# Optimization experiments

Measured on AMD Instinct MI355X. Metric: run time of the kernel, lower is better.

The kernel has to match this reference:

```python
import jax, jax.numpy as jnp
import numpy as np

EPS = 1e-12  # F.normalize eps


def setup_inputs() -> dict:
    key = jax.random.key(0)
    k1, k2, k3, k4 = jax.random.split(key, 4)
    D, K, H, W = 256, 64, 512, 512
    x = jax.random.normal(k1, (1, D, H, W), dtype=jnp.float32)
    c = jax.random.normal(k2, (K, D), dtype=jnp.float32)
    conv_w = jax.random.normal(k3, (K, D), dtype=jnp.float32) * (1.0 / np.sqrt(D))
    conv_b = jax.random.normal(k4, (K,), dtype=jnp.float32) * 0.01
    return {"x": x, "c": c, "conv_w": conv_w, "conv_b": conv_b}


def reference(x, c, conv_w, conv_b):
    # x: (1, D, H, W); base_cnn treated as identity (feature map given directly)
    _, D, H, W = x.shape
    K = conv_w.shape[0]
    N = H * W
    xf = x.reshape(D, N)                                  # (D, N) local descriptors

    # 1x1 conv soft-assignment: logits (K, N), softmax over clusters K
    logits = jnp.einsum('kd,dn->kn', conv_w, xf) + conv_b[:, None]
    a_bar = jax.nn.softmax(logits, axis=0)                # (K, N)

    # VLAD core (vectorized): V[k] = sum_n a_bar[k,n] * (x[:,n] - c[k])
    V = jnp.einsum('kn,dn->kd', a_bar, xf) - c * a_bar.sum(axis=1, keepdims=True)  # (K, D)

    # intra-normalization over cluster axis (dim=0), then per-row L2 (F.normalize default dim=1)
    V = V / jnp.maximum(jnp.linalg.norm(V, axis=0, keepdims=True), EPS)
    y = V / jnp.maximum(jnp.linalg.norm(V, axis=1, keepdims=True), EPS)
    return y
```

## Files before the change

### kernel.cpp

```cpp
#include <hip/hip_runtime.h>
#include <hip/hip_bf16.h>

#define DD    256
#define KK    64
#define NPIX  262144
#define NW    128
#define NWIN  8
#define GRID  256
#define BLOCK 512

#define W_S   264
#define XT_S  132
#define AB_S  136
#define XC_S  40
#define SV_S  257

typedef __attribute__((ext_vector_type(8))) short bf16x8;
typedef __attribute__((ext_vector_type(4))) float f32x4;

union Frag { bf16x8 v; int i[4]; };

__device__ __forceinline__ int cvtpk(float a, float b) {
    __hip_bfloat162 h = __float22bfloat162_rn(float2{a, b});
    int r; __builtin_memcpy(&r, &h, 4); return r;
}

__device__ __forceinline__ void lds_barrier() {
    asm volatile("s_waitcnt lgkmcnt(0)" ::: "memory");
    __builtin_amdgcn_s_barrier();
}

__global__ __attribute__((amdgpu_flat_work_group_size(BLOCK, BLOCK), amdgpu_waves_per_eu(2, 2)))
void netvlad_fused(const float* __restrict__ x, const float* __restrict__ conv_w,
                   const float* __restrict__ conv_b, float* __restrict__ Vpart,
                   float* __restrict__ asum_part)
{
    __shared__ short Wl[KK * W_S];
    __shared__ short Ab[KK * AB_S];
    __shared__ float asb[8][KK];
    __shared__ short slice_mem[8 * 16 * XC_S];
    __shared__ union {
        short xt[DD * XT_S];
        float sv[KK * SV_S];
    } UX;

    const int t    = threadIdx.x;
    const int lane = t & 63;
    const int w    = t >> 6;
    const int l15  = lane & 15;
    const int q    = (lane >> 4) & 3;
    const int bid  = blockIdx.x;
    const size_t n0 = (size_t)bid * (NWIN * NW);

    const int p  = lane >> 2;
    const int ng = lane & 3;
    const size_t nself0 = n0 + 16 * w + 4 * ng;

    float4 pr[4][2];
    #pragma unroll
    for (int c = 0; c < 2; ++c)
        #pragma unroll
        for (int j = 0; j < 2; ++j)
            pr[c][j] = *(const float4*)(x + (size_t)(32 * c + 2 * p + j) * NPIX + nself0);
    __builtin_amdgcn_sched_barrier(0);

    #pragma unroll
    for (int i = 0; i < 32; ++i) {
        int idx = t + BLOCK * i;
        float wv = conv_w[idx];
        __hip_bfloat16 hb = __float2bfloat16(wv);
        short s; __builtin_memcpy(&s, &hb, 2);
        Wl[(idx >> 8) * W_S + (idx & 255)] = s;
    }

    #pragma unroll
    for (int c = 2; c < 4; ++c)
        #pragma unroll
        for (int j = 0; j < 2; ++j)
            pr[c][j] = *(const float4*)(x + (size_t)(32 * c + 2 * p + j) * NPIX + nself0);
    __builtin_amdgcn_sched_barrier(0);

    float breg[4][4];
    #pragma unroll
    for (int mt = 0; mt < 4; ++mt)
        #pragma unroll
        for (int r = 0; r < 4; ++r)
            breg[mt][r] = conv_b[16 * mt + 4 * q + r];

    f32x4 acc[2][4];
    #pragma unroll
    for (int rg = 0; rg < 2; ++rg)
        #pragma unroll
        for (int ct = 0; ct < 4; ++ct)
            acc[rg][ct] = (f32x4){0.f, 0.f, 0.f, 0.f};
    float asumReg = 0.f;

    short* slice = &slice_mem[w * (16 * XC_S)];

    lds_barrier();

    for (int i = 0; i < NWIN; ++i) {
        const size_t nselfw = n0 + (size_t)i * NW + 16 * w + 4 * ng;

        f32x4 Lc[4];
        #pragma unroll
        for (int mt = 0; mt < 4; ++mt) Lc[mt] = (f32x4){0.f, 0.f, 0.f, 0.f};

        #pragma unroll
        for (int ch = 0; ch < 8; ++ch) {
            const int cur = ch & 3;
            const float* r0 = (const float*)&pr[cur][0];
            const float* r1 = (const float*)&pr[cur][1];

            #pragma unroll
            for (int c = 0; c < 4; ++c) {
                int pk = cvtpk(r0[c], r1[c]);
                *(int*)&slice[(4 * ng + c) * XC_S + 2 * p] = pk;
            }
            {
                int2 a; a.x = cvtpk(r0[0], r0[1]); a.y = cvtpk(r0[2], r0[3]);
                *(int2*)&UX.xt[(32 * ch + 2 * p) * XT_S + 16 * w + 4 * ng] = a;
                int2 b; b.x = cvtpk(r1[0], r1[1]); b.y = cvtpk(r1[2], r1[3]);
                *(int2*)&UX.xt[(32 * ch + 2 * p + 1) * XT_S + 16 * w + 4 * ng] = b;
            }

            if (ch < 4) {
                #pragma unroll
                for (int j = 0; j < 2; ++j)
                    pr[cur][j] = *(const float4*)(x + (size_t)(32 * (ch + 4) + 2 * p + j) * NPIX + nselfw);
                __builtin_amdgcn_sched_barrier(0);
            } else if (i + 1 < NWIN) {
                #pragma unroll
                for (int j = 0; j < 2; ++j)
                    pr[cur][j] = *(const float4*)(x + (size_t)(32 * (ch - 4) + 2 * p + j) * NPIX + nselfw + NW);
                __builtin_amdgcn_sched_barrier(0);
            }

            Frag Bv = *(const Frag*)&slice[l15 * XC_S + 8 * q];
            #pragma unroll
            for (int mt = 0; mt < 4; ++mt) {
                Frag A = *(const Frag*)&Wl[(16 * mt + l15) * W_S + 32 * ch + 8 * q];
                Lc[mt] = __builtin_amdgcn_mfma_f32_16x16x32_bf16(A.v, Bv.v, Lc[mt], 0, 0, 0);
            }
        }

        {
            float mx = -1e30f;
            #pragma unroll
            for (int mt = 0; mt < 4; ++mt)
                #pragma unroll
                for (int r = 0; r < 4; ++r) {
                    Lc[mt][r] += breg[mt][r];
                    mx = fmaxf(mx, Lc[mt][r]);
                }
            mx = fmaxf(mx, __shfl_xor(mx, 16));
            mx = fmaxf(mx, __shfl_xor(mx, 32));
            float s = 0.f;
            #pragma unroll
            for (int mt = 0; mt < 4; ++mt)
                #pragma unroll
                for (int r = 0; r < 4; ++r) {
                    float e = __expf(Lc[mt][r] - mx);
                    Lc[mt][r] = e;
                    s += e;
                }
            s += __shfl_xor(s, 16);
            s += __shfl_xor(s, 32);
            float inv = 1.0f / s;
            #pragma unroll
            for (int mt = 0; mt < 4; ++mt)
                #pragma unroll
                for (int r = 0; r < 4; ++r)
                    Lc[mt][r] *= inv;
        }

        #pragma unroll
        for (int mt = 0; mt < 4; ++mt)
            #pragma unroll
            for (int r = 0; r < 4; ++r) {
                float v = Lc[mt][r];
                v += __shfl_xor(v, 1);
                v += __shfl_xor(v, 2);
                v += __shfl_xor(v, 4);
                v += __shfl_xor(v, 8);
                if (l15 == 0) asb[w][16 * mt + 4 * q + r] = v;
            }

        #pragma unroll
        for (int mt = 0; mt < 4; ++mt)
            #pragma unroll
            for (int r = 0; r < 4; ++r) {
                __hip_bfloat16 hb = __float2bfloat16(Lc[mt][r]);
                short sv_; __builtin_memcpy(&sv_, &hb, 2);
                Ab[(16 * mt + 4 * q + r) * AB_S + 16 * w + l15] = sv_;
            }

        lds_barrier();

        if (t < KK) {
            float s = 0.f;
            #pragma unroll
            for (int ww = 0; ww < 8; ++ww) s += asb[ww][t];
            asumReg += s;
        }

        #pragma unroll
        for (int s = 0; s < 4; ++s) {
            Frag Af0 = *(const Frag*)&UX.xt[(32 * w + l15) * XT_S + 32 * s + 8 * q];
            Frag Af1 = *(const Frag*)&UX.xt[(32 * w + 16 + l15) * XT_S + 32 * s + 8 * q];
            Frag Bf[4];
            #pragma unroll
            for (int ct = 0; ct < 4; ++ct)
                Bf[ct] = *(const Frag*)&Ab[(16 * ct + l15) * AB_S + 32 * s + 8 * q];
            #pragma unroll
            for (int ct = 0; ct < 4; ++ct) {
                acc[0][ct] = __builtin_amdgcn_mfma_f32_16x16x32_bf16(Af0.v, Bf[ct].v, acc[0][ct], 0, 0, 0);
                acc[1][ct] = __builtin_amdgcn_mfma_f32_16x16x32_bf16(Af1.v, Bf[ct].v, acc[1][ct], 0, 0, 0);
            }
        }

        lds_barrier();
    }

    if (t < KK) asum_part[(size_t)bid * KK + t] = asumReg;

    #pragma unroll
    for (int rg = 0; rg < 2; ++rg)
        #pragma unroll
        for (int ct = 0; ct < 4; ++ct)
            #pragma unroll
            for (int r = 0; r < 4; ++r) {
                int k = 16 * ct + l15;
                int d = 32 * w + 16 * rg + 4 * q + r;
                UX.sv[k * SV_S + d] = acc[rg][ct][r];
            }
    __syncthreads();

    float* vout = Vpart + (size_t)bid * (KK * DD);
    #pragma unroll
    for (int ii = 0; ii < 32; ++ii) {
        int idx = t + BLOCK * ii;
        vout[idx] = UX.sv[(idx >> 8) * SV_S + (idx & 255)];
    }
}

__global__ __launch_bounds__(256)
void netvlad_reduce(const float* __restrict__ Vpart, const float* __restrict__ asum_part,
                    float* __restrict__ Vred, float* __restrict__ asum_red)
{
    __shared__ float sbuf[256];
    const int t = threadIdx.x;
    if (blockIdx.x < 256) {
        const int o = blockIdx.x * 64 + (t & 63);
        const int g = t >> 6;
        float s = 0.f;
        #pragma unroll 8
        for (int i = 0; i < 64; ++i)
            s += Vpart[(size_t)(g * 64 + i) * (KK * DD) + o];
        sbuf[t] = s;
        __syncthreads();
        if (t < 64) Vred[o] = sbuf[t] + sbuf[t + 64] + sbuf[t + 128] + sbuf[t + 192];
    } else {
        const int k = t & 63;
        const int g = t >> 6;
        float s = 0.f;
        #pragma unroll 8
        for (int i = 0; i < 64; ++i)
            s += asum_part[(size_t)(g * 64 + i) * KK + k];
        sbuf[t] = s;
        __syncthreads();
        if (t < 64) asum_red[k] = sbuf[t] + sbuf[t + 64] + sbuf[t + 128] + sbuf[t + 192];
    }
}

__global__ __launch_bounds__(1024)
void netvlad_finalize(const float* __restrict__ Vws, const float* __restrict__ asum_ws,
                      const float* __restrict__ c, float* __restrict__ y)
{
    __shared__ float sV[KK * DD];
    __shared__ float sa[KK];
    __shared__ float colf[DD];
    __shared__ float rowf[KK];
    const int t = threadIdx.x;

    if (t < KK) sa[t] = asum_ws[t];
    __syncthreads();

    #pragma unroll
    for (int i = 0; i < 16; ++i) {
        int idx = t + 1024 * i;
        sV[idx] = Vws[idx] - c[idx] * sa[idx >> 8];
    }
    __syncthreads();

    if (t < DD) {
        float s = 0.f;
        for (int k = 0; k < KK; ++k) { float v = sV[k * DD + t]; s += v * v; }
        colf[t] = 1.0f / fmaxf(sqrtf(s), 1e-12f);
    }
    __syncthreads();

    #pragma unroll
    for (int i = 0; i < 16; ++i) {
        int idx = t + 1024 * i;
        sV[idx] *= colf[idx & 255];
    }
    __syncthreads();

    {
        int k = t >> 4, p = t & 15;
        float s = 0.f;
        #pragma unroll
        for (int j = 0; j < 16; ++j) { float v = sV[k * DD + p + 16 * j]; s += v * v; }
        s += __shfl_xor(s, 1);
        s += __shfl_xor(s, 2);
        s += __shfl_xor(s, 4);
        s += __shfl_xor(s, 8);
        if (p == 0) rowf[k] = 1.0f / fmaxf(sqrtf(s), 1e-12f);
    }
    __syncthreads();

    #pragma unroll
    for (int i = 0; i < 16; ++i) {
        int idx = t + 1024 * i;
        y[idx] = sV[idx] * rowf[idx >> 8];
    }
}

extern "C" void kernel_launch(void* const* d_in, const int* in_sizes, int n_in,
                              void* d_out, int out_size, void* d_ws, size_t ws_size,
                              hipStream_t stream) {
    const float* x      = (const float*)d_in[0];
    const float* c      = (const float*)d_in[1];
    const float* conv_w = (const float*)d_in[2];
    const float* conv_b = (const float*)d_in[3];
    float* y = (float*)d_out;

    float* Vpart     = (float*)d_ws;
    float* asum_part = Vpart + (size_t)GRID * KK * DD;
    float* Vred      = asum_part + (size_t)GRID * KK;
    float* asum_red  = Vred + KK * DD;

    netvlad_fused<<<GRID, BLOCK, 0, stream>>>(x, conv_w, conv_b, Vpart, asum_part);
    netvlad_reduce<<<257, 256, 0, stream>>>(Vpart, asum_part, Vred, asum_red);
    netvlad_finalize<<<1, 1024, 0, stream>>>(Vred, asum_red, c, y);
}
```

Baseline: 84.61 us.

## Double-buffer assignment tile and prefetch xt fragments to release barrier early

The per-window softmax assignment tile Ab is double-buffered by window parity. The xt A-fragments are loaded into registers before a barrier, and the second-stage MFMAs run after it, so the next window's xt writes can start while this window's aggregation MFMAs are still running. The conv weight is also pre-swizzled in LDS into MFMA fragment order, so each lane reads a contiguous 16 bytes, with float4 global loads during staging. The cost is more LDS for the second Ab buffer and more registers for the prefetched fragments, under a two-waves-per-EU occupancy target.

Measured after the change: 85.10 us. No clear change (+0.6%).

```diff
diff --git a/kernel.cpp b/kernel.cpp
--- a/kernel.cpp
+++ b/kernel.cpp
@@ -9,7 +9,6 @@
 #define GRID  256
 #define BLOCK 512
 
-#define W_S   264
 #define XT_S  132
 #define AB_S  136
 #define XC_S  40
@@ -35,8 +34,8 @@
                    const float* __restrict__ conv_b, float* __restrict__ Vpart,
                    float* __restrict__ asum_part)
 {
-    __shared__ short Wl[KK * W_S];
-    __shared__ short Ab[KK * AB_S];
+    __shared__ short Wf[4 * 8 * 64 * 8];
+    __shared__ short Ab[2][KK * AB_S];
     __shared__ float asb[8][KK];
     __shared__ short slice_mem[8 * 16 * XC_S];
     __shared__ union {
@@ -65,12 +64,18 @@
     __builtin_amdgcn_sched_barrier(0);
 
     #pragma unroll
-    for (int i = 0; i < 32; ++i) {
-        int idx = t + BLOCK * i;
-        float wv = conv_w[idx];
-        __hip_bfloat16 hb = __float2bfloat16(wv);
-        short s; __builtin_memcpy(&s, &hb, 2);
-        Wl[(idx >> 8) * W_S + (idx & 255)] = s;
+    for (int i = 0; i < 8; ++i) {
+        int u = t + BLOCK * i;
+        int S = 4 * u;
+        int e4 = S & 7;
+        int ln = (S >> 3) & 63;
+        int ch = (S >> 9) & 7;
+        int mt = S >> 12;
+        int k  = 16 * mt + (ln & 15);
+        int d  = 32 * ch + 8 * ((ln >> 4) & 3) + e4;
+        float4 wv = *(const float4*)(conv_w + k * DD + d);
+        int2 pk; pk.x = cvtpk(wv.x, wv.y); pk.y = cvtpk(wv.z, wv.w);
+        *(int2*)&Wf[S] = pk;
     }
 
     #pragma unroll
@@ -100,6 +105,7 @@
     lds_barrier();
 
     for (int i = 0; i < NWIN; ++i) {
+        const int ib = i & 1;
         const size_t nselfw = n0 + (size_t)i * NW + 16 * w + 4 * ng;
 
         f32x4 Lc[4];
@@ -139,7 +145,7 @@
             Frag Bv = *(const Frag*)&slice[l15 * XC_S + 8 * q];
             #pragma unroll
             for (int mt = 0; mt < 4; ++mt) {
-                Frag A = *(const Frag*)&Wl[(16 * mt + l15) * W_S + 32 * ch + 8 * q];
+                Frag A = *(const Frag*)&Wf[(((mt << 3) + ch) << 9) + (lane << 3)];
                 Lc[mt] = __builtin_amdgcn_mfma_f32_16x16x32_bf16(A.v, Bv.v, Lc[mt], 0, 0, 0);
             }
         }
@@ -192,7 +198,7 @@
             for (int r = 0; r < 4; ++r) {
                 __hip_bfloat16 hb = __float2bfloat16(Lc[mt][r]);
                 short sv_; __builtin_memcpy(&sv_, &hb, 2);
-                Ab[(16 * mt + 4 * q + r) * AB_S + 16 * w + l15] = sv_;
+                Ab[ib][(16 * mt + 4 * q + r) * AB_S + 16 * w + l15] = sv_;
             }
 
         lds_barrier();
@@ -204,22 +210,27 @@
             asumReg += s;
         }
 
+        Frag Afp[2][4];
         #pragma unroll
         for (int s = 0; s < 4; ++s) {
-            Frag Af0 = *(const Frag*)&UX.xt[(32 * w + l15) * XT_S + 32 * s + 8 * q];
-            Frag Af1 = *(const Frag*)&UX.xt[(32 * w + 16 + l15) * XT_S + 32 * s + 8 * q];
+            Afp[0][s] = *(const Frag*)&UX.xt[(32 * w + l15) * XT_S + 32 * s + 8 * q];
+            Afp[1][s] = *(const Frag*)&UX.xt[(32 * w + 16 + l15) * XT_S + 32 * s + 8 * q];
+        }
+
+        lds_barrier();
+
+        #pragma unroll
+        for (int s = 0; s < 4; ++s) {
             Frag Bf[4];
             #pragma unroll
             for (int ct = 0; ct < 4; ++ct)
-                Bf[ct] = *(const Frag*)&Ab[(16 * ct + l15) * AB_S + 32 * s + 8 * q];
+                Bf[ct] = *(const Frag*)&Ab[ib][(16 * ct + l15) * AB_S + 32 * s + 8 * q];
             #pragma unroll
             for (int ct = 0; ct < 4; ++ct) {
-                acc[0][ct] = __builtin_amdgcn_mfma_f32_16x16x32_bf16(Af0.v, Bf[ct].v, acc[0][ct], 0, 0, 0);
-                acc[1][ct] = __builtin_amdgcn_mfma_f32_16x16x32_bf16(Af1.v, Bf[ct].v, acc[1][ct], 0, 0, 0);
-            }
-        }
-
-        lds_barrier();
+                acc[0][ct] = __builtin_amdgcn_mfma_f32_16x16x32_bf16(Afp[0][s].v, Bf[ct].v, acc[0][ct], 0, 0, 0);
+                acc[1][ct] = __builtin_amdgcn_mfma_f32_16x16x32_bf16(Afp[1][s].v, Bf[ct].v, acc[1][ct], 0, 0, 0);
+            }
+        }
     }
 
     if (t < KK) asum_part[(size_t)bid * KK + t] = asumReg;
```

## Fuse reduce and finalize kernels using last-block atomic counter

Applied to the files above, without the earlier changes.

Merges the partial-sum reduction and the single-block normalization into one kernel. Each block reduces its slice of partial VLAD sums, then an atomic counter picks the last block to finish, which sums the assignment weights and runs the intra and L2 normalization. This removes one kernel launch and its gap, but adds a memset launch, and the finalize now runs on 256 threads instead of 1024 with a serial per-row norm loop.

New measurement: 114.1 us. +34.8%, slower.

```diff
diff --git a/kernel.cpp b/kernel.cpp
--- a/kernel.cpp
+++ b/kernel.cpp
@@ -245,84 +245,73 @@
 }
 
 __global__ __launch_bounds__(256)
-void netvlad_reduce(const float* __restrict__ Vpart, const float* __restrict__ asum_part,
-                    float* __restrict__ Vred, float* __restrict__ asum_red)
+void netvlad_reduce_finalize(const float* __restrict__ Vpart, const float* __restrict__ asum_part,
+                             float* __restrict__ Vred, const float* __restrict__ c,
+                             float* __restrict__ y, unsigned int* __restrict__ done)
 {
     __shared__ float sbuf[256];
     const int t = threadIdx.x;
-    if (blockIdx.x < 256) {
-        const int o = blockIdx.x * 64 + (t & 63);
-        const int g = t >> 6;
-        float s = 0.f;
-        #pragma unroll 8
-        for (int i = 0; i < 64; ++i)
-            s += Vpart[(size_t)(g * 64 + i) * (KK * DD) + o];
-        sbuf[t] = s;
-        __syncthreads();
-        if (t < 64) Vred[o] = sbuf[t] + sbuf[t + 64] + sbuf[t + 128] + sbuf[t + 192];
-    } else {
-        const int k = t & 63;
-        const int g = t >> 6;
-        float s = 0.f;
-        #pragma unroll 8
-        for (int i = 0; i < 64; ++i)
-            s += asum_part[(size_t)(g * 64 + i) * KK + k];
-        sbuf[t] = s;
-        __syncthreads();
-        if (t < 64) asum_red[k] = sbuf[t] + sbuf[t + 64] + sbuf[t + 128] + sbuf[t + 192];
-    }
-}
-
-__global__ __launch_bounds__(1024)
-void netvlad_finalize(const float* __restrict__ Vws, const float* __restrict__ asum_ws,
-                      const float* __restrict__ c, float* __restrict__ y)
-{
+
+    const int o = blockIdx.x * 64 + (t & 63);
+    const int g = t >> 6;
+    float s = 0.f;
+    #pragma unroll 8
+    for (int i = 0; i < 64; ++i)
+        s += Vpart[(size_t)(g * 64 + i) * (KK * DD) + o];
+    sbuf[t] = s;
+    __syncthreads();
+    if (t < 64) Vred[o] = sbuf[t] + sbuf[t + 64] + sbuf[t + 128] + sbuf[t + 192];
+
+    __shared__ unsigned int lastFlag;
+    __threadfence();
+    if (t == 0) lastFlag = (atomicAdd(done, 1u) == (GRID - 1));
+    __syncthreads();
+    if (!lastFlag) return;
+    __threadfence();
+
+    __shared__ float sa[KK];
+    if (t < KK) {
+        float a = 0.f;
+        for (int i = 0; i < GRID; ++i) a += asum_part[(size_t)i * KK + t];
+        sa[t] = a;
+    }
+
     __shared__ float sV[KK * DD];
-    __shared__ float sa[KK];
     __shared__ float colf[DD];
     __shared__ float rowf[KK];
-    const int t = threadIdx.x;
-
-    if (t < KK) sa[t] = asum_ws[t];
-    __syncthreads();
-
-    #pragma unroll
-    for (int i = 0; i < 16; ++i) {
-        int idx = t + 1024 * i;
-        sV[idx] = Vws[idx] - c[idx] * sa[idx >> 8];
-    }
-    __syncthreads();
-
-    if (t < DD) {
-        float s = 0.f;
-        for (int k = 0; k < KK; ++k) { float v = sV[k * DD + t]; s += v * v; }
-        colf[t] = 1.0f / fmaxf(sqrtf(s), 1e-12f);
-    }
-    __syncthreads();
-
-    #pragma unroll
-    for (int i = 0; i < 16; ++i) {
-        int idx = t + 1024 * i;
+    __syncthreads();
+
+    #pragma unroll 8
+    for (int i = 0; i < 64; ++i) {
+        int idx = t + 256 * i;
+        sV[idx] = Vred[idx] - c[idx] * sa[idx >> 8];
+    }
+    __syncthreads();
+
+    {
+        float ss = 0.f;
+        for (int k = 0; k < KK; ++k) { float v = sV[k * DD + t]; ss += v * v; }
+        colf[t] = 1.0f / fmaxf(sqrtf(ss), 1e-12f);
+    }
+    __syncthreads();
+
+    #pragma unroll 8
+    for (int i = 0; i < 64; ++i) {
+        int idx = t + 256 * i;
         sV[idx] *= colf[idx & 255];
     }
     __syncthreads();
 
-    {
-        int k = t >> 4, p = t & 15;
-        float s = 0.f;
-        #pragma unroll
-        for (int j = 0; j < 16; ++j) { float v = sV[k * DD + p + 16 * j]; s += v * v; }
-        s += __shfl_xor(s, 1);
-        s += __shfl_xor(s, 2);
-        s += __shfl_xor(s, 4);
-        s += __shfl_xor(s, 8);
-        if (p == 0) rowf[k] = 1.0f / fmaxf(sqrtf(s), 1e-12f);
-    }
-    __syncthreads();
-
-    #pragma unroll
-    for (int i = 0; i < 16; ++i) {
-        int idx = t + 1024 * i;
+    if (t < KK) {
+        float ss = 0.f;
+        for (int j = 0; j < DD; ++j) { float v = sV[t * DD + j]; ss += v * v; }
+        rowf[t] = 1.0f / fmaxf(sqrtf(ss), 1e-12f);
+    }
+    __syncthreads();
+
+    #pragma unroll 8
+    for (int i = 0; i < 64; ++i) {
+        int idx = t + 256 * i;
         y[idx] = sV[idx] * rowf[idx >> 8];
     }
 }
@@ -339,9 +328,9 @@
     float* Vpart     = (float*)d_ws;
     float* asum_part = Vpart + (size_t)GRID * KK * DD;
     float* Vred      = asum_part + (size_t)GRID * KK;
-    float* asum_red  = Vred + KK * DD;
-
+    unsigned int* done = (unsigned int*)(Vred + KK * DD);
+
+    hipMemsetAsync(done, 0, sizeof(unsigned int), stream);
     netvlad_fused<<<GRID, BLOCK, 0, stream>>>(x, conv_w, conv_b, Vpart, asum_part);
-    netvlad_reduce<<<257, 256, 0, stream>>>(Vpart, asum_part, Vred, asum_red);
-    netvlad_finalize<<<1, 1024, 0, stream>>>(Vred, asum_red, c, y);
-}
+    netvlad_reduce_finalize<<<GRID, 256, 0, stream>>>(Vpart, asum_part, Vred, c, y, done);
+}
```
